# Performance work log

Hardware: AMD Instinct MI355X
Metric: run time of the kernel (lower is better)

## Reference

```python
import jax, jax.numpy as jnp
import numpy as np

V, E, H, L, C = 30000, 512, 256, 2, 16  # vocab, embed, lstm hidden, layers, tags
B, S = 32, 512
NH, HD = 2, (2 * H) // 2  # attention heads, head dim


def setup_inputs() -> dict:
    key = jax.random.key(0)
    ks = jax.random.split(key, 16)
    s = 0.05
    return {
        "x": jax.random.randint(ks[0], (B, S), 0, V),
        "labels": jax.random.randint(ks[1], (B, S), 0, C),
        "emb": jax.random.normal(ks[2], (V, E), jnp.float32) * s,
        # stacked LSTM params: [layer, dir, ...]; layer0 in=E=512, layer1 in=2H=512
        "lstm_wih": jax.random.normal(ks[3], (L, 2, 4 * H, E), jnp.float32) * s,
        "lstm_whh": jax.random.normal(ks[4], (L, 2, 4 * H, H), jnp.float32) * s,
        "lstm_bih": jax.random.normal(ks[5], (L, 2, 4 * H), jnp.float32) * s,
        "lstm_bhh": jax.random.normal(ks[6], (L, 2, 4 * H), jnp.float32) * s,
        "in_proj_w": jax.random.normal(ks[7], (3 * 2 * H, 2 * H), jnp.float32) * s,
        "in_proj_b": jax.random.normal(ks[8], (3 * 2 * H,), jnp.float32) * s,
        "out_proj_w": jax.random.normal(ks[9], (2 * H, 2 * H), jnp.float32) * s,
        "out_proj_b": jax.random.normal(ks[10], (2 * H,), jnp.float32) * s,
        "fc_w": jax.random.normal(ks[11], (C, 2 * H), jnp.float32) * s,
        "fc_b": jax.random.normal(ks[12], (C,), jnp.float32) * s,
        "crf_start": jax.random.normal(ks[13], (C,), jnp.float32) * s,
        "crf_end": jax.random.normal(ks[14], (C,), jnp.float32) * s,
        "crf_trans": jax.random.normal(ks[15], (C, C), jnp.float32) * s,
    }


def _lstm_dir(x_sbf, wih, whh, b, reverse):
    # x_sbf: [S, B, F]; PyTorch gate order i, f, g, o
    h0 = jnp.zeros((x_sbf.shape[1], whh.shape[1]), x_sbf.dtype)

    def step(carry, xt):
        h, c = carry
        z = xt @ wih.T + h @ whh.T + b
        i, f, g, o = jnp.split(z, 4, axis=-1)
        c = jax.nn.sigmoid(f) * c + jax.nn.sigmoid(i) * jnp.tanh(g)
        h = jax.nn.sigmoid(o) * jnp.tanh(c)
        return (h, c), h

    _, hs = jax.lax.scan(step, (h0, h0), x_sbf, reverse=reverse)
    return hs  # [S, B, H], aligned to input time order


def _bilstm(x, lstm_wih, lstm_whh, lstm_bih, lstm_bhh):
    # x: [B, S, E] -> [B, S, 2H]; dropout between layers skipped (eval)
    h = jnp.swapaxes(x, 0, 1)  # [S, B, E]
    for l in range(L):
        b_f = lstm_bih[l, 0] + lstm_bhh[l, 0]
        b_b = lstm_bih[l, 1] + lstm_bhh[l, 1]
        fwd = _lstm_dir(h, lstm_wih[l, 0], lstm_whh[l, 0], b_f, False)
        bwd = _lstm_dir(h, lstm_wih[l, 1], lstm_whh[l, 1], b_b, True)
        h = jnp.concatenate([fwd, bwd], axis=-1)  # [S, B, 2H]
    return jnp.swapaxes(h, 0, 1)  # [B, S, 2H]


def _mha(x, in_proj_w, in_proj_b, out_proj_w, out_proj_b):
    # Faithful to the source bug: nn.MultiheadAttention (seq-first) is fed
    # batch-first data, so axis 0 (batch B) is the attention/sequence axis
    # and axis 1 (S) acts as the batch. x: [B, S, 2H]
    qkv = x @ in_proj_w.T + in_proj_b
    q, k, v = jnp.split(qkv, 3, axis=-1)
    q = q.reshape(B, S, NH, HD)
    k = k.reshape(B, S, NH, HD)
    v = v.reshape(B, S, NH, HD)
    scores = jnp.einsum('lshd,mshd->hslm', q, k) / np.sqrt(HD).astype(np.float32)
    attn = jax.nn.softmax(scores, axis=-1)
    out = jnp.einsum('hslm,mshd->lshd', attn, v).reshape(B, S, 2 * H)
    return out @ out_proj_w.T + out_proj_b


def _crf_nll(emissions, tags, crf_start, crf_end, crf_trans):
    # torchcrf log-likelihood, full mask, reduction='sum'; returns -llh
    em = jnp.swapaxes(emissions, 0, 1)   # [S, B, C]
    tg = jnp.swapaxes(tags, 0, 1)        # [S, B]
    bidx = jnp.arange(B)

    # numerator: score of the gold path
    score0 = crf_start[tg[0]] + em[0, bidx, tg[0]]

    def num_step(score, xs):
        em_t, tp, tt = xs
        return score + crf_trans[tp, tt] + em_t[bidx, tt], None

    score, _ = jax.lax.scan(num_step, score0, (em[1:], tg[:-1], tg[1:]))
    score = score + crf_end[tg[-1]]

    # denominator: forward algorithm (logsumexp recurrence)
    alpha0 = crf_start[None, :] + em[0]  # [B, C]

    def fwd_step(alpha, em_t):
        nxt = jax.nn.logsumexp(alpha[:, :, None] + crf_trans[None] + em_t[:, None, :], axis=1)
        return nxt, None

    alpha, _ = jax.lax.scan(fwd_step, alpha0, em[1:])
    logZ = jax.nn.logsumexp(alpha + crf_end[None, :], axis=1)

    llh = jnp.sum(score - logZ)
    return -llh


def reference(x, labels, emb, lstm_wih, lstm_whh, lstm_bih, lstm_bhh,
              in_proj_w, in_proj_b, out_proj_w, out_proj_b,
              fc_w, fc_b, crf_start, crf_end, crf_trans):
    e = emb[x]                                              # [B, S, E]
    h = _bilstm(e, lstm_wih, lstm_whh, lstm_bih, lstm_bhh)  # [B, S, 2H]
    a = _mha(h, in_proj_w, in_proj_b, out_proj_w, out_proj_b)
    logits = a @ fc_w.T + fc_b                              # [B, S, C]
    nll = _crf_nll(logits, labels, crf_start, crf_end, crf_trans)
    return logits, nll
```

## Files before the change

kernel.cpp:

```cpp
#include <hip/hip_runtime.h>
#include <hip/hip_bf16.h>
#include <cstdint>

#define S_ 512
#define B_ 32
#define E_ 512
#define H_ 256
#define C_ 16

typedef float f32x4_t __attribute__((ext_vector_type(4)));
typedef __bf16 bf16x8_t __attribute__((ext_vector_type(8)));

__device__ __forceinline__ float bf2f(unsigned short u) {
    return __uint_as_float(((unsigned int)u) << 16);
}
__device__ __forceinline__ unsigned short f2bf(float f) {
    unsigned int u = __float_as_uint(f);
    unsigned int r = (u + 0x7FFFu + ((u >> 16) & 1u)) >> 16;
    return (unsigned short)r;
}
__device__ __forceinline__ float sigf(float x) { return 1.f / (1.f + __expf(-x)); }
__device__ __forceinline__ float tanhf_fast(float x) {
    float e = __expf(-2.f * fabsf(x));
    float r = (1.f - e) / (1.f + e);
    return x >= 0.f ? r : -r;
}

__global__ __launch_bounds__(128) void embed_gather(
    const int* __restrict__ x, const float* __restrict__ emb, unsigned short* __restrict__ X)
{
    int row = blockIdx.x;
    int s = row >> 5, b = row & 31;
    int idx = x[b * S_ + s];
    float4 v = ((const float4*)(emb + (size_t)idx * E_))[threadIdx.x];
    ushort4 o; o.x = f2bf(v.x); o.y = f2bf(v.y); o.z = f2bf(v.z); o.w = f2bf(v.w);
    ((ushort4*)(X + (size_t)row * E_))[threadIdx.x] = o;
}

__global__ __launch_bounds__(256) void conv_f2b(
    const float* __restrict__ src, unsigned short* __restrict__ dst, int n)
{
    int i = (blockIdx.x * 256 + threadIdx.x) * 4;
    if (i < n) {
        float4 v = *(const float4*)(src + i);
        ushort4 o; o.x = f2bf(v.x); o.y = f2bf(v.y); o.z = f2bf(v.z); o.w = f2bf(v.w);
        *(ushort4*)(dst + i) = o;
    }
}

template<int STORE_MODE>
__global__ __launch_bounds__(256) void gemm_bf16(
    const unsigned short* __restrict__ A, const unsigned short* __restrict__ W,
    const float* __restrict__ b1, const float* __restrict__ b2,
    void* __restrict__ Cout, int M, int N, int K)
{
    __shared__ __align__(16) char lds[16384];
    char* asb = lds;
    char* wsb = lds + 8192;
    const int tid = threadIdx.x;
    const int m0 = blockIdx.x * 64, n0 = blockIdx.y * 64;
    const int w = tid >> 6, L = tid & 63;
    const int sr = tid >> 2, sq = tid & 3;
    const int mrow = L & 15, kg = (L >> 4) * 8;
    f32x4_t acc[4];
    #pragma unroll
    for (int ni = 0; ni < 4; ++ni) acc[ni] = f32x4_t{0.f, 0.f, 0.f, 0.f};

    for (int k0 = 0; k0 < K; k0 += 64) {
        uint4 av1 = *(const uint4*)(A + (size_t)(m0 + sr) * K + k0 + sq * 16);
        uint4 av2 = *(const uint4*)(A + (size_t)(m0 + sr) * K + k0 + sq * 16 + 8);
        uint4 wv1 = *(const uint4*)(W + (size_t)(n0 + sr) * K + k0 + sq * 16);
        uint4 wv2 = *(const uint4*)(W + (size_t)(n0 + sr) * K + k0 + sq * 16 + 8);
        __syncthreads();
        int sw = (sr & 7) << 4;
        *(uint4*)(asb + ((sr * 128 + sq * 32) ^ sw))      = av1;
        *(uint4*)(asb + ((sr * 128 + sq * 32 + 16) ^ sw)) = av2;
        *(uint4*)(wsb + ((sr * 128 + sq * 32) ^ sw))      = wv1;
        *(uint4*)(wsb + ((sr * 128 + sq * 32 + 16) ^ sw)) = wv2;
        __syncthreads();
        #pragma unroll
        for (int kb = 0; kb < 2; ++kb) {
            int kl = kb * 32 + kg;
            int ar = w * 16 + mrow;
            bf16x8_t a = *(const bf16x8_t*)(asb + ((ar * 128 + kl * 2) ^ ((ar & 7) << 4)));
            #pragma unroll
            for (int ni = 0; ni < 4; ++ni) {
                int nr = ni * 16 + mrow;
                bf16x8_t b = *(const bf16x8_t*)(wsb + ((nr * 128 + kl * 2) ^ ((nr & 7) << 4)));
                acc[ni] = __builtin_amdgcn_mfma_f32_16x16x32_bf16(a, b, acc[ni], 0, 0, 0);
            }
        }
    }
    #pragma unroll
    for (int ni = 0; ni < 4; ++ni) {
        int n = n0 + ni * 16 + mrow;
        float bb = (b1 ? b1[n] : 0.f) + (b2 ? b2[n] : 0.f);
        #pragma unroll
        for (int r = 0; r < 4; ++r) {
            int m = m0 + w * 16 + (L >> 4) * 4 + r;
            float v = acc[ni][r] + bb;
            if (STORE_MODE == 2) {
                int tq = m >> 5, b = m & 31;
                ((unsigned short*)Cout)[((size_t)tq * N + n) * 32 + b] = f2bf(v);
            } else if (STORE_MODE == 1) {
                ((unsigned short*)Cout)[(size_t)m * N + n] = f2bf(v);
            } else {
                ((float*)Cout)[(size_t)m * N + n] = v;
            }
        }
    }
}

__global__ __launch_bounds__(512, 2) void lstm_rec5(
    const unsigned short* __restrict__ Zf,
    const unsigned short* __restrict__ Zb,
    const unsigned short* __restrict__ whhb,
    unsigned short* __restrict__ Hb)
{
    __shared__ __align__(16) char lds[163840];
    const int tid = threadIdx.x;
    const int d  = blockIdx.x >> 1;
    const int bh = blockIdx.x & 1;
    const int w = tid >> 6, L = tid & 63;
    const int lr = L & 15;
    const int kq = L >> 4;
    const int kg8 = kq * 8;
    const unsigned short* Z = d ? Zb : Zf;
    const unsigned short* Wd = whhb + (size_t)d * 262144;
    const int hbase = 155648;

    for (int i = 0; i < 16; ++i) {
        int c = i * 512 + tid;
        int row = c >> 3, seg = c & 7;
        uint4 v = *(const uint4*)(Wd + (size_t)row * 256 + seg * 8);
        *(uint4*)(lds + ((row * 128 + seg * 16) ^ ((row & 7) << 4))) = v;
    }
    for (int i = 0; i < 3; ++i) {
        int c = i * 512 + tid;
        int rB = c >> 2, seg = c & 3;
        int g = rB >> 7, rem = rB & 127;
        int grow = g * 256 + (rem >> 4) * 32 + (rem & 15);
        uint4 v = *(const uint4*)(Wd + (size_t)grow * 256 + 64 + seg * 8);
        *(uint4*)(lds + 131072 + ((rB * 64 + seg * 16) ^ ((rB & 3) << 4))) = v;
    }
    bf16x8_t wr[5][4][2];
    #pragma unroll
    for (int kk = 0; kk < 5; ++kk)
        #pragma unroll
        for (int g = 0; g < 4; ++g)
            #pragma unroll
            for (int jt = 0; jt < 2; ++jt)
                wr[kk][g][jt] = *(const bf16x8_t*)(
                    Wd + (size_t)(g * 256 + w * 32 + jt * 16 + lr) * 256 + (kk + 3) * 32 + kg8);
    bf16x8_t wk2_j1[4];
    #pragma unroll
    for (int g = 0; g < 4; ++g)
        wk2_j1[g] = *(const bf16x8_t*)(
            Wd + (size_t)(g * 256 + w * 32 + 16 + lr) * 256 + 64 + kg8);
    bf16x8_t wk2_j0g3 = *(const bf16x8_t*)(
        Wd + (size_t)(3 * 256 + w * 32 + lr) * 256 + 64 + kg8);

    float cst[2][4] = {{0.f, 0.f, 0.f, 0.f}, {0.f, 0.f, 0.f, 0.f}};
    __syncthreads();

    for (int tt = 0; tt < 512; ++tt) {
        const int t = d ? (511 - tt) : tt;

        f32x4_t acc[4][2];
        #pragma unroll
        for (int g = 0; g < 4; ++g)
            #pragma unroll
            for (int jt = 0; jt < 2; ++jt) {
                ushort4 z = *(const ushort4*)(
                    Z + (size_t)t * 32768 + (g * 256 + w * 32 + jt * 16 + lr) * 32 + bh * 16 + kq * 4);
                acc[g][jt] = f32x4_t{bf2f(z.x), bf2f(z.y), bf2f(z.z), bf2f(z.w)};
            }

        if (tt > 0) {
            #pragma unroll
            for (int kt = 0; kt < 8; ++kt) {
                bf16x8_t af = *(const bf16x8_t*)(
                    lds + hbase + ((lr * 512 + (kt * 32 + kg8) * 2) ^ ((lr & 7) << 4)));
                #pragma unroll
                for (int g = 0; g < 4; ++g)
                    #pragma unroll
                    for (int jt = 0; jt < 2; ++jt) {
                        bf16x8_t bf;
                        if (kt < 2) {
                            int row = g * 256 + w * 32 + jt * 16 + lr;
                            bf = *(const bf16x8_t*)(
                                lds + ((row * 128 + (kt * 32 + kg8) * 2) ^ ((row & 7) << 4)));
                        } else if (kt == 2) {
                            if (jt == 0 && g < 3) {
                                int rB = g * 128 + w * 16 + lr;
                                bf = *(const bf16x8_t*)(
                                    lds + 131072 + ((rB * 64 + kg8 * 2) ^ ((rB & 3) << 4)));
                            } else if (jt == 0) {
                                bf = wk2_j0g3;
                            } else {
                                bf = wk2_j1[g];
                            }
                        } else {
                            bf = wr[kt - 3][g][jt];
                        }
                        acc[g][jt] = __builtin_amdgcn_mfma_f32_16x16x32_bf16(af, bf, acc[g][jt], 0, 0, 0);
                    }
            }
        }

        __syncthreads();

        #pragma unroll
        for (int jt = 0; jt < 2; ++jt) {
            const int u = w * 32 + jt * 16 + lr;
            #pragma unroll
            for (int r = 0; r < 4; ++r) {
                float iv = sigf(acc[0][jt][r]);
                float fv = sigf(acc[1][jt][r]);
                float gv = tanhf_fast(acc[2][jt][r]);
                float ov = sigf(acc[3][jt][r]);
                float c = fv * cst[jt][r] + iv * gv;
                cst[jt][r] = c;
                float hh = ov * tanhf_fast(c);
                unsigned short hb = f2bf(hh);
                int bl = kq * 4 + r;
                *(unsigned short*)(lds + hbase + ((bl * 512 + u * 2) ^ ((bl & 7) << 4))) = hb;
                Hb[((size_t)t * 32 + bh * 16 + bl) * 512 + d * 256 + u] = hb;
            }
        }
        __syncthreads();
    }
}

__global__ __launch_bounds__(256) void attn_fused(
    const unsigned short* __restrict__ qkv, unsigned short* __restrict__ outp)
{
    int s = blockIdx.x & 511;
    int h = blockIdx.x >> 9;
    __shared__ float qs[32][260];
    __shared__ float ks[32][260];
    __shared__ float vs[32][260];
    __shared__ float sc[32][36];
    int tid = threadIdx.x;
    for (int it = 0; it < 32; ++it) {
        const unsigned short* base = qkv + ((size_t)s * 32 + it) * 1536 + h * 256 + tid;
        qs[it][tid] = bf2f(base[0]);
        ks[it][tid] = bf2f(base[512]);
        vs[it][tid] = bf2f(base[1024]);
    }
    __syncthreads();
    int l = tid >> 3, m0 = (tid & 7) * 4;
    float a0 = 0, a1 = 0, a2 = 0, a3 = 0;
    for (int dd = 0; dd < 256; dd += 4) {
        float4 q4 = *(const float4*)&qs[l][dd];
        float4 k0v = *(const float4*)&ks[m0 + 0][dd];
        float4 k1v = *(const float4*)&ks[m0 + 1][dd];
        float4 k2v = *(const float4*)&ks[m0 + 2][dd];
        float4 k3v = *(const float4*)&ks[m0 + 3][dd];
        a0 += q4.x * k0v.x + q4.y * k0v.y + q4.z * k0v.z + q4.w * k0v.w;
        a1 += q4.x * k1v.x + q4.y * k1v.y + q4.z * k1v.z + q4.w * k1v.w;
        a2 += q4.x * k2v.x + q4.y * k2v.y + q4.z * k2v.z + q4.w * k2v.w;
        a3 += q4.x * k3v.x + q4.y * k3v.y + q4.z * k3v.z + q4.w * k3v.w;
    }
    sc[l][m0 + 0] = a0 * 0.0625f;
    sc[l][m0 + 1] = a1 * 0.0625f;
    sc[l][m0 + 2] = a2 * 0.0625f;
    sc[l][m0 + 3] = a3 * 0.0625f;
    __syncthreads();
    if (tid < 32) {
        float mx = -1e30f;
        for (int m = 0; m < 32; ++m) mx = fmaxf(mx, sc[tid][m]);
        float pr[32]; float sm = 0.f;
        for (int m = 0; m < 32; ++m) { pr[m] = __expf(sc[tid][m] - mx); sm += pr[m]; }
        float inv = 1.f / sm;
        for (int m = 0; m < 32; ++m) sc[tid][m] = pr[m] * inv;
    }
    __syncthreads();
    int l2 = tid >> 3, d0 = (tid & 7) * 32;
    float o[32] = {};
    for (int m = 0; m < 32; ++m) {
        float aw = sc[l2][m];
        #pragma unroll
        for (int dd = 0; dd < 32; dd += 4) {
            float4 v4 = *(const float4*)&vs[m][d0 + dd];
            o[dd] += aw * v4.x; o[dd + 1] += aw * v4.y; o[dd + 2] += aw * v4.z; o[dd + 3] += aw * v4.w;
        }
    }
    unsigned short* ob = outp + ((size_t)s * 32 + l2) * 512 + h * 256 + d0;
    #pragma unroll
    for (int dd = 0; dd < 32; dd += 4) {
        ushort4 pv;
        pv.x = f2bf(o[dd]); pv.y = f2bf(o[dd + 1]); pv.z = f2bf(o[dd + 2]); pv.w = f2bf(o[dd + 3]);
        *(ushort4*)(ob + dd) = pv;
    }
}

__global__ __launch_bounds__(256) void fc_logits(
    const float* __restrict__ A, const float* __restrict__ fcw, const float* __restrict__ fcb,
    float* __restrict__ outp)
{
    __shared__ float wsm[16][516];
    int tid = threadIdx.x;
    for (int idx = tid; idx < 8192; idx += 256) wsm[idx >> 9][idx & 511] = fcw[idx];
    __syncthreads();
    int r = blockIdx.x * 16 + (tid >> 4);
    int c = tid & 15;
    const float* ar = A + (size_t)r * 512;
    float acc = 0.f;
    for (int k = 0; k < 512; k += 4) {
        float4 a4 = *(const float4*)(ar + k);
        float4 w4 = *(const float4*)&wsm[c][k];
        acc += a4.x * w4.x + a4.y * w4.y + a4.z * w4.z + a4.w * w4.w;
    }
    int s = r >> 5, b = r & 31;
    outp[(size_t)b * 8192 + s * 16 + c] = acc + fcb[c];
}

__global__ __launch_bounds__(256) void crf_forward(
    const float* __restrict__ em, const int* __restrict__ labels,
    const float* __restrict__ cs, const float* __restrict__ ce, const float* __restrict__ ct,
    float* __restrict__ res)
{
    int b = blockIdx.x;
    int tid = threadIdx.x;
    int jj = tid >> 4, ii = tid & 15;
    __shared__ float trans[16][17];
    __shared__ float alpha[2][16];
    __shared__ float red[256];
    trans[tid >> 4][tid & 15] = ct[tid & 255];
    const float* emb_ = em + (size_t)b * 8192;
    const int* tg = labels + b * 512;
    float part = 0.f;
    for (int t = tid; t < 512; t += 256) {
        int cur = tg[t];
        part += emb_[t * 16 + cur] + (t == 0 ? cs[cur] : ct[tg[t - 1] * 16 + cur]);
    }
    red[tid] = part;
    if (tid < 16) alpha[0][tid] = cs[tid] + emb_[tid];
    __syncthreads();
    for (int off = 128; off > 0; off >>= 1) {
        if (tid < off) red[tid] += red[tid + off];
        __syncthreads();
    }
    for (int t = 1; t < 512; ++t) {
        int p = t & 1;
        float v = alpha[p ^ 1][ii] + trans[ii][jj];
        float mx = v;
        mx = fmaxf(mx, __shfl_xor(mx, 1));
        mx = fmaxf(mx, __shfl_xor(mx, 2));
        mx = fmaxf(mx, __shfl_xor(mx, 4));
        mx = fmaxf(mx, __shfl_xor(mx, 8));
        float e = __expf(v - mx);
        e += __shfl_xor(e, 1); e += __shfl_xor(e, 2); e += __shfl_xor(e, 4); e += __shfl_xor(e, 8);
        if (ii == 0) alpha[p][jj] = mx + __logf(e) + emb_[t * 16 + jj];
        __syncthreads();
    }
    if (tid == 0) {
        float mx = -1e30f;
        for (int c2 = 0; c2 < 16; ++c2) mx = fmaxf(mx, alpha[1][c2] + ce[c2]);
        float sm = 0.f;
        for (int c2 = 0; c2 < 16; ++c2) sm += __expf(alpha[1][c2] + ce[c2] - mx);
        float logZ = mx + __logf(sm);
        float score = red[0] + ce[tg[511]];
        res[b] = logZ - score;
    }
}

__global__ void crf_final(const float* __restrict__ res, float* __restrict__ nll)
{
    if (threadIdx.x == 0) {
        float s2 = 0.f;
        for (int b = 0; b < 32; ++b) s2 += res[b];
        nll[0] = s2;
    }
}

extern "C" void kernel_launch(void* const* d_in, const int* in_sizes, int n_in,
                              void* d_out, int out_size, void* d_ws, size_t ws_size,
                              hipStream_t stream)
{
    const int* x      = (const int*)d_in[0];
    const int* labels = (const int*)d_in[1];
    const float* emb  = (const float*)d_in[2];
    const float* wih  = (const float*)d_in[3];
    const float* whh  = (const float*)d_in[4];
    const float* bih  = (const float*)d_in[5];
    const float* bhh  = (const float*)d_in[6];
    const float* inw  = (const float*)d_in[7];
    const float* inb  = (const float*)d_in[8];
    const float* opw  = (const float*)d_in[9];
    const float* opb  = (const float*)d_in[10];
    const float* fcw  = (const float*)d_in[11];
    const float* fcb  = (const float*)d_in[12];
    const float* cs   = (const float*)d_in[13];
    const float* ce   = (const float*)d_in[14];
    const float* ct   = (const float*)d_in[15];
    float* out = (float*)d_out;

    char* ws = (char*)d_ws;
    const size_t MiB = 1ull << 20;
    unsigned short* Xb    = (unsigned short*)(ws);
    unsigned short* attnO = (unsigned short*)(ws);
    unsigned short* H0b   = (unsigned short*)(ws + 16 * MiB);
    float*          OPout = (float*)(ws + 16 * MiB);
    float*          res   = (float*)(ws + 16 * MiB);
    unsigned short* H1b   = (unsigned short*)(ws + 32 * MiB);
    unsigned short* Zfb   = (unsigned short*)(ws + 48 * MiB);
    unsigned short* qkv   = (unsigned short*)(ws + 48 * MiB);
    unsigned short* Zbb   = (unsigned short*)(ws + 80 * MiB);
    unsigned short* wihb  = (unsigned short*)(ws + 112 * MiB);
    unsigned short* whhb  = (unsigned short*)(ws + 116 * MiB);
    unsigned short* inwb  = (unsigned short*)(ws + 118 * MiB);
    unsigned short* opwb  = (unsigned short*)(ws + 119 * MiB + 512 * 1024);

    embed_gather<<<16384, 128, 0, stream>>>(x, emb, Xb);
    conv_f2b<<<2048, 256, 0, stream>>>(wih, wihb, 2097152);
    conv_f2b<<<1024, 256, 0, stream>>>(whh, whhb, 1048576);
    conv_f2b<<<768, 256, 0, stream>>>(inw, inwb, 786432);
    conv_f2b<<<256, 256, 0, stream>>>(opw, opwb, 262144);

    for (int l = 0; l < 2; ++l) {
        const unsigned short* Ain = l ? H0b : Xb;
        unsigned short* Ho        = l ? H1b : H0b;
        for (int dd = 0; dd < 2; ++dd) {
            gemm_bf16<2><<<dim3(256, 16), 256, 0, stream>>>(
                Ain, wihb + (size_t)(l * 2 + dd) * 524288,
                bih + (l * 2 + dd) * 1024, bhh + (l * 2 + dd) * 1024,
                dd ? (void*)Zbb : (void*)Zfb, 16384, 1024, 512);
        }
        lstm_rec5<<<4, 512, 0, stream>>>(Zfb, Zbb, whhb + (size_t)l * 524288, Ho);
    }

    gemm_bf16<1><<<dim3(256, 24), 256, 0, stream>>>(H1b, inwb, inb, nullptr, (void*)qkv, 16384, 1536, 512);
    attn_fused<<<1024, 256, 0, stream>>>(qkv, attnO);
    gemm_bf16<0><<<dim3(256, 8), 256, 0, stream>>>(attnO, opwb, opb, nullptr, (void*)OPout, 16384, 512, 512);

    fc_logits<<<1024, 256, 0, stream>>>(OPout, fcw, fcb, out);

    crf_forward<<<32, 256, 0, stream>>>(out, labels, cs, ce, ct, res);
    crf_final<<<1, 64, 0, stream>>>(res, out + 262144);

    (void)in_sizes; (void)n_in; (void)out_size; (void)ws_size;
}
```

Baseline: 6.176 ms.

## Double LSTM recurrence block to 1024 threads, one 16-unit tile per wave

The recurrent LSTM kernel now runs with 1024 threads (16 waves) per block instead of 512. Each wave handles 16 hidden units instead of 32, which halves the per-thread MFMA chain and the register-resident weight slices on the serial per-step critical path. The split between LDS-held and register-held W_hh tiles is rebalanced for the new mapping, shrinking the LDS footprint. The cost is more waves contending at the two per-step barriers and tighter register limits at 1024 threads, which could cause spills.

After: 6.841 ms. +10.8%, slower.

```diff
diff --git a/kernel.cpp b/kernel.cpp
--- a/kernel.cpp
+++ b/kernel.cpp
@@ -111,13 +111,13 @@
     }
 }
 
-__global__ __launch_bounds__(512, 2) void lstm_rec5(
+__global__ __launch_bounds__(1024) void lstm_rec8(
     const unsigned short* __restrict__ Zf,
     const unsigned short* __restrict__ Zb,
     const unsigned short* __restrict__ whhb,
     unsigned short* __restrict__ Hb)
 {
-    __shared__ __align__(16) char lds[163840];
+    __shared__ __align__(16) char lds[155648];
     const int tid = threadIdx.x;
     const int d  = blockIdx.x >> 1;
     const int bh = blockIdx.x & 1;
@@ -125,56 +125,47 @@
     const int lr = L & 15;
     const int kq = L >> 4;
     const int kg8 = kq * 8;
+    const int u  = w * 16 + lr;
     const unsigned short* Z = d ? Zb : Zf;
     const unsigned short* Wd = whhb + (size_t)d * 262144;
-    const int hbase = 155648;
-
-    for (int i = 0; i < 16; ++i) {
-        int c = i * 512 + tid;
+    const int hbase = 147456;
+
+    for (int i = 0; i < 8; ++i) {
+        int c = i * 1024 + tid;
         int row = c >> 3, seg = c & 7;
         uint4 v = *(const uint4*)(Wd + (size_t)row * 256 + seg * 8);
         *(uint4*)(lds + ((row * 128 + seg * 16) ^ ((row & 7) << 4))) = v;
     }
-    for (int i = 0; i < 3; ++i) {
-        int c = i * 512 + tid;
-        int rB = c >> 2, seg = c & 3;
-        int g = rB >> 7, rem = rB & 127;
-        int grow = g * 256 + (rem >> 4) * 32 + (rem & 15);
-        uint4 v = *(const uint4*)(Wd + (size_t)grow * 256 + 64 + seg * 8);
+    {
+        int rB = tid >> 2, seg = tid & 3;
+        uint4 v = *(const uint4*)(Wd + (size_t)rB * 256 + 64 + seg * 8);
         *(uint4*)(lds + 131072 + ((rB * 64 + seg * 16) ^ ((rB & 3) << 4))) = v;
     }
-    bf16x8_t wr[5][4][2];
+    bf16x8_t wr[5][4];
     #pragma unroll
     for (int kk = 0; kk < 5; ++kk)
         #pragma unroll
         for (int g = 0; g < 4; ++g)
-            #pragma unroll
-            for (int jt = 0; jt < 2; ++jt)
-                wr[kk][g][jt] = *(const bf16x8_t*)(
-                    Wd + (size_t)(g * 256 + w * 32 + jt * 16 + lr) * 256 + (kk + 3) * 32 + kg8);
-    bf16x8_t wk2_j1[4];
+            wr[kk][g] = *(const bf16x8_t*)(
+                Wd + (size_t)(g * 256 + u) * 256 + (kk + 3) * 32 + kg8);
+    bf16x8_t wk2[3];
     #pragma unroll
-    for (int g = 0; g < 4; ++g)
-        wk2_j1[g] = *(const bf16x8_t*)(
-            Wd + (size_t)(g * 256 + w * 32 + 16 + lr) * 256 + 64 + kg8);
-    bf16x8_t wk2_j0g3 = *(const bf16x8_t*)(
-        Wd + (size_t)(3 * 256 + w * 32 + lr) * 256 + 64 + kg8);
-
-    float cst[2][4] = {{0.f, 0.f, 0.f, 0.f}, {0.f, 0.f, 0.f, 0.f}};
+    for (int g = 1; g < 4; ++g)
+        wk2[g - 1] = *(const bf16x8_t*)(Wd + (size_t)(g * 256 + u) * 256 + 64 + kg8);
+
+    f32x4_t cst = f32x4_t{0.f, 0.f, 0.f, 0.f};
     __syncthreads();
 
     for (int tt = 0; tt < 512; ++tt) {
         const int t = d ? (511 - tt) : tt;
 
-        f32x4_t acc[4][2];
-        #pragma unroll
-        for (int g = 0; g < 4; ++g)
-            #pragma unroll
-            for (int jt = 0; jt < 2; ++jt) {
-                ushort4 z = *(const ushort4*)(
-                    Z + (size_t)t * 32768 + (g * 256 + w * 32 + jt * 16 + lr) * 32 + bh * 16 + kq * 4);
-                acc[g][jt] = f32x4_t{bf2f(z.x), bf2f(z.y), bf2f(z.z), bf2f(z.w)};
-            }
+        f32x4_t acc[4];
+        #pragma unroll
+        for (int g = 0; g < 4; ++g) {
+            ushort4 z = *(const ushort4*)(
+                Z + (size_t)t * 32768 + (g * 256 + u) * 32 + bh * 16 + kq * 4);
+            acc[g] = f32x4_t{bf2f(z.x), bf2f(z.y), bf2f(z.z), bf2f(z.w)};
+        }
 
         if (tt > 0) {
             #pragma unroll
@@ -182,51 +173,42 @@
                 bf16x8_t af = *(const bf16x8_t*)(
                     lds + hbase + ((lr * 512 + (kt * 32 + kg8) * 2) ^ ((lr & 7) << 4)));
                 #pragma unroll
-                for (int g = 0; g < 4; ++g)
-                    #pragma unroll
-                    for (int jt = 0; jt < 2; ++jt) {
-                        bf16x8_t bf;
-                        if (kt < 2) {
-                            int row = g * 256 + w * 32 + jt * 16 + lr;
+                for (int g = 0; g < 4; ++g) {
+                    bf16x8_t bf;
+                    if (kt < 2) {
+                        int row = g * 256 + u;
+                        bf = *(const bf16x8_t*)(
+                            lds + ((row * 128 + (kt * 32 + kg8) * 2) ^ ((row & 7) << 4)));
+                    } else if (kt == 2) {
+                        if (g == 0) {
                             bf = *(const bf16x8_t*)(
-                                lds + ((row * 128 + (kt * 32 + kg8) * 2) ^ ((row & 7) << 4)));
-                        } else if (kt == 2) {
-                            if (jt == 0 && g < 3) {
-                                int rB = g * 128 + w * 16 + lr;
-                                bf = *(const bf16x8_t*)(
-                                    lds + 131072 + ((rB * 64 + kg8 * 2) ^ ((rB & 3) << 4)));
-                            } else if (jt == 0) {
-                                bf = wk2_j0g3;
-                            } else {
-                                bf = wk2_j1[g];
-                            }
+                                lds + 131072 + ((u * 64 + kg8 * 2) ^ ((u & 3) << 4)));
                         } else {
-                            bf = wr[kt - 3][g][jt];
+                            bf = wk2[g - 1];
                         }
-                        acc[g][jt] = __builtin_amdgcn_mfma_f32_16x16x32_bf16(af, bf, acc[g][jt], 0, 0, 0);
+                    } else {
+                        bf = wr[kt - 3][g];
                     }
+                    acc[g] = __builtin_amdgcn_mfma_f32_16x16x32_bf16(af, bf, acc[g], 0, 0, 0);
+                }
             }
         }
 
         __syncthreads();
 
         #pragma unroll
-        for (int jt = 0; jt < 2; ++jt) {
-            const int u = w * 32 + jt * 16 + lr;
-            #pragma unroll
-            for (int r = 0; r < 4; ++r) {
-                float iv = sigf(acc[0][jt][r]);
-                float fv = sigf(acc[1][jt][r]);
-                float gv = tanhf_fast(acc[2][jt][r]);
-                float ov = sigf(acc[3][jt][r]);
-                float c = fv * cst[jt][r] + iv * gv;
-                cst[jt][r] = c;
-                float hh = ov * tanhf_fast(c);
-                unsigned short hb = f2bf(hh);
-                int bl = kq * 4 + r;
-                *(unsigned short*)(lds + hbase + ((bl * 512 + u * 2) ^ ((bl & 7) << 4))) = hb;
-                Hb[((size_t)t * 32 + bh * 16 + bl) * 512 + d * 256 + u] = hb;
-            }
+        for (int r = 0; r < 4; ++r) {
+            float iv = sigf(acc[0][r]);
+            float fv = sigf(acc[1][r]);
+            float gv = tanhf_fast(acc[2][r]);
+            float ov = sigf(acc[3][r]);
+            float c = fv * cst[r] + iv * gv;
+            cst[r] = c;
+            float hh = ov * tanhf_fast(c);
+            unsigned short hb = f2bf(hh);
+            int bl = kq * 4 + r;
+            *(unsigned short*)(lds + hbase + ((bl * 512 + u * 2) ^ ((bl & 7) << 4))) = hb;
+            Hb[((size_t)t * 32 + bh * 16 + bl) * 512 + d * 256 + u] = hb;
         }
         __syncthreads();
     }
@@ -428,7 +410,7 @@
                 bih + (l * 2 + dd) * 1024, bhh + (l * 2 + dd) * 1024,
                 dd ? (void*)Zbb : (void*)Zfb, 16384, 1024, 512);
         }
-        lstm_rec5<<<4, 512, 0, stream>>>(Zfb, Zbb, whhb + (size_t)l * 524288, Ho);
+        lstm_rec8<<<4, 1024, 0, stream>>>(Zfb, Zbb, whhb + (size_t)l * 524288, Ho);
     }
 
     gemm_bf16<1><<<dim3(256, 24), 256, 0, stream>>>(H1b, inwb, inb, nullptr, (void*)qkv, 16384, 1536, 512);
```
